# Kernel optimization log

Hardware: AMD Instinct MI355X
Metric: run time of the kernel (lower is better)

Reference implementation:

```python
import jax, jax.numpy as jnp
import numpy as np

N = 8192
EPS = 1e-7  # matches torch BCE's internal log clamping behavior


def setup_inputs() -> dict:
    key = jax.random.key(0)
    ks = jax.random.split(key, 8)
    return {
        "solar_score": jax.random.normal(ks[0], (N,), dtype=jnp.float32),
        "solar_ranking_gt": jax.random.randint(ks[1], (N,), 0, 1000000, dtype=jnp.int64),
        "capacity_pred": jax.random.normal(ks[2], (N,), dtype=jnp.float32),
        "capacity_gt": jax.random.normal(ks[3], (N,), dtype=jnp.float32),
        "roi_pred": jax.random.normal(ks[4], (N,), dtype=jnp.float32),
        "roi_gt": jax.random.normal(ks[5], (N,), dtype=jnp.float32),
        "viable_pred": jax.random.uniform(ks[6], (N,), dtype=jnp.float32, minval=1e-4, maxval=1.0 - 1e-4),
        "viable_gt": jax.random.uniform(ks[7], (N,), dtype=jnp.float32),
    }


def _pairwise_ranking_loss(scores, gt_ranking):
    n = scores.shape[0]
    # pair (i, j) with i < j contributes iff gt_ranking[i] < gt_ranking[j]
    upper = jnp.triu(jnp.ones((n, n), dtype=bool), k=1)
    mask = (gt_ranking[:, None] < gt_ranking[None, :]) & upper
    hinge = jax.nn.relu(1.0 - (scores[:, None] - scores[None, :]))  # [n, n]
    count = jnp.sum(mask)
    total = jnp.sum(jnp.where(mask, hinge, 0.0))
    return jnp.where(count > 0, total / count.astype(scores.dtype), jnp.zeros((), scores.dtype))


def reference(solar_score, solar_ranking_gt, capacity_pred, capacity_gt,
              roi_pred, roi_gt, viable_pred, viable_gt):
    ranking_loss = _pairwise_ranking_loss(solar_score, solar_ranking_gt)

    capacity_loss = jnp.mean((capacity_pred - capacity_gt) ** 2)

    d = roi_pred - roi_gt  # smooth_l1 with beta=1 (torch default)
    ad = jnp.abs(d)
    roi_loss = jnp.mean(jnp.where(ad < 1.0, 0.5 * d * d, ad - 0.5))

    p = jnp.clip(viable_pred, EPS, 1.0 - EPS)
    viability_loss = -jnp.mean(viable_gt * jnp.log(p) + (1.0 - viable_gt) * jnp.log1p(-p))

    return (ranking_loss + capacity_loss + roi_loss + viability_loss) / 4.0
```

## Files before the change

### kernel.cpp

```cpp
#include <hip/hip_runtime.h>

#define NELEM 8192
#define NPAIR 1024
#define NTHREADS 512
#define JTILE (NTHREADS * 4)
#define EPSV 1e-7f
#define TAG16   0xA5C3u
#define MAGIC32 0xA5C3F17Du

__global__ __launch_bounds__(NTHREADS, 4) void solar_fused_kernel(
    const float* __restrict__ s, const int* __restrict__ r,
    const float* __restrict__ cp, const float* __restrict__ cg,
    const float* __restrict__ rp, const float* __restrict__ rg,
    const float* __restrict__ vp, const float* __restrict__ vg,
    unsigned long long* __restrict__ pw, float* __restrict__ out) {

    const int b   = blockIdx.x;
    const int tid = threadIdx.x;

    __shared__ float    rft[NTHREADS / 64];
    __shared__ float    rfe[NTHREADS / 64];
    __shared__ unsigned rcu[NTHREADS / 64];
    __shared__ double   dd[NTHREADS / 64];
    __shared__ unsigned cc[NTHREADS / 64];
    __shared__ float    fe[NTHREADS / 64];

    const int joff = tid * 4;
    const int i0a = 4 * b;
    const int i0b = 8188 - 4 * b;

    const float4 sa4 = *reinterpret_cast<const float4*>(s + i0a);
    const int4   ra4 = *reinterpret_cast<const int4*>(r + i0a);
    const float4 sb4 = *reinterpret_cast<const float4*>(s + i0b);
    const int4   rb4 = *reinterpret_cast<const int4*>(r + i0b);
    const float4 c1a = make_float4(1.0f - sa4.x, 1.0f - sa4.y, 1.0f - sa4.z, 1.0f - sa4.w);
    const float4 c1b = make_float4(1.0f - sb4.x, 1.0f - sb4.y, 1.0f - sb4.z, 1.0f - sb4.w);

    float    tacc[4] = {0.0f, 0.0f, 0.0f, 0.0f};
    unsigned cnt_u   = 0;

    auto comp_full = [&](float4 sj, int4 rj, float4 c1, int4 ri) {
        const float c1e[4] = {c1.x, c1.y, c1.z, c1.w};
        const int   rie[4] = {ri.x, ri.y, ri.z, ri.w};
        const float sje[4] = {sj.x, sj.y, sj.z, sj.w};
        const int   rje[4] = {rj.x, rj.y, rj.z, rj.w};
#pragma unroll
        for (int k = 0; k < 4; ++k) {
#pragma unroll
            for (int e = 0; e < 4; ++e) {
                const bool cond = rie[k] < rje[e];
                const float h = fmaxf(0.0f, c1e[k] + sje[e]);
                tacc[e] += cond ? h : 0.0f;
                cnt_u += (unsigned)__popcll(__ballot(cond));
            }
        }
    };

    auto comp_diag = [&](float4 sj, int4 rj, float4 c1, int4 ri, int jb, int i0) {
        const float c1e[4] = {c1.x, c1.y, c1.z, c1.w};
        const int   rie[4] = {ri.x, ri.y, ri.z, ri.w};
        const float sje[4] = {sj.x, sj.y, sj.z, sj.w};
        const int   rje[4] = {rj.x, rj.y, rj.z, rj.w};
#pragma unroll
        for (int k = 0; k < 4; ++k) {
#pragma unroll
            for (int e = 0; e < 4; ++e) {
                const bool cond = ((jb + e) > (i0 + k)) & (rie[k] < rje[e]);
                const float h = fmaxf(0.0f, c1e[k] + sje[e]);
                tacc[e] += cond ? h : 0.0f;
                cnt_u += (unsigned)__popcll(__ballot(cond));
            }
        }
    };

    if (b < 512) {
        const int jb0 = joff, jb1 = JTILE + joff, jb2 = 2 * JTILE + joff, jb3 = 3 * JTILE + joff;
        const float4 s1 = *reinterpret_cast<const float4*>(s + jb1);
        const float4 s2 = *reinterpret_cast<const float4*>(s + jb2);
        const float4 s3 = *reinterpret_cast<const float4*>(s + jb3);
        const int4   r1 = *reinterpret_cast<const int4*>(r + jb1);
        const int4   r2 = *reinterpret_cast<const int4*>(r + jb2);
        const int4   r3 = *reinterpret_cast<const int4*>(r + jb3);

        comp_full(s1, r1, c1a, ra4);
        comp_full(s2, r2, c1a, ra4);
        comp_full(s3, r3, c1a, ra4);

        if (__any((jb0 + 3) > i0a)) {
            const float4 s0 = *reinterpret_cast<const float4*>(s + jb0);
            const int4   r0 = *reinterpret_cast<const int4*>(r + jb0);
            comp_diag(s0, r0, c1a, ra4, jb0, i0a);
        }
        if (__any((jb3 + 3) > i0b)) {
            comp_diag(s3, r3, c1b, rb4, jb3, i0b);
        }
    } else {
        const int jb1 = JTILE + joff, jb2 = 2 * JTILE + joff, jb3 = 3 * JTILE + joff;
        const float4 s2 = *reinterpret_cast<const float4*>(s + jb2);
        const float4 s3 = *reinterpret_cast<const float4*>(s + jb3);
        const int4   r2 = *reinterpret_cast<const int4*>(r + jb2);
        const int4   r3 = *reinterpret_cast<const int4*>(r + jb3);

        comp_full(s2, r2, c1a, ra4);
        comp_full(s3, r3, c1a, ra4);
        comp_full(s3, r3, c1b, rb4);

        if (__any((jb1 + 3) > i0a)) {
            const float4 s1 = *reinterpret_cast<const float4*>(s + jb1);
            const int4   r1 = *reinterpret_cast<const int4*>(r + jb1);
            comp_diag(s1, r1, c1a, ra4, jb1, i0a);
        }
        if (__any((jb2 + 3) > i0b)) {
            comp_diag(s2, r2, c1b, rb4, jb2, i0b);
        }
    }

    float ext = 0.0f;
    if (tid < 8) {
        const int i = b * 8 + tid;
        const float dc = cp[i] - cg[i];
        const float cap = dc * dc;
        const float dr = rp[i] - rg[i];
        const float ad = fabsf(dr);
        const float roi = (ad < 1.0f) ? 0.5f * dr * dr : (ad - 0.5f);
        const float p = fminf(fmaxf(vp[i], EPSV), 1.0f - EPSV);
        const float g = vg[i];
        const float bce = g * logf(p) + (1.0f - g) * log1pf(-p);
        ext = cap + roi - bce;
    }

    float tsum = (tacc[0] + tacc[1]) + (tacc[2] + tacc[3]);
#pragma unroll
    for (int off = 32; off > 0; off >>= 1) {
        tsum += __shfl_down(tsum, off);
        ext  += __shfl_down(ext,  off);
    }

    const int wave = tid >> 6;
    const int lane = tid & 63;
    if (lane == 0) { rft[wave] = tsum; rfe[wave] = ext; rcu[wave] = cnt_u; }
    __syncthreads();

    if (tid == 0) {
        float bt = 0.0f, be = 0.0f;
        unsigned bc = 0;
#pragma unroll
        for (int w = 0; w < NTHREADS / 64; ++w) { bt += rft[w]; be += rfe[w]; bc += rcu[w]; }
        const unsigned long long w0 =
            ((unsigned long long)((TAG16 << 16) | (bc & 0xFFFFu)) << 32) | (unsigned long long)__float_as_uint(bt);
        const unsigned long long w1 =
            ((unsigned long long)MAGIC32 << 32) | (unsigned long long)__float_as_uint(be);
        __hip_atomic_store(&pw[2 * b],     w0, __ATOMIC_RELAXED, __HIP_MEMORY_SCOPE_AGENT);
        __hip_atomic_store(&pw[2 * b + 1], w1, __ATOMIC_RELAXED, __HIP_MEMORY_SCOPE_AGENT);
    }

    if (b == 0) {
        double   td = 0.0;
        unsigned cn = 0;
        float    ex = 0.0f;
#pragma unroll
        for (int q = 0; q < 2; ++q) {
            const int blk = tid + q * NTHREADS;
            unsigned long long w0 = __hip_atomic_load(&pw[2 * blk], __ATOMIC_RELAXED, __HIP_MEMORY_SCOPE_AGENT);
            while ((unsigned)(w0 >> 48) != TAG16) {
                __builtin_amdgcn_s_sleep(2);
                w0 = __hip_atomic_load(&pw[2 * blk], __ATOMIC_RELAXED, __HIP_MEMORY_SCOPE_AGENT);
            }
            unsigned long long w1 = __hip_atomic_load(&pw[2 * blk + 1], __ATOMIC_RELAXED, __HIP_MEMORY_SCOPE_AGENT);
            while ((unsigned)(w1 >> 32) != MAGIC32) {
                __builtin_amdgcn_s_sleep(2);
                w1 = __hip_atomic_load(&pw[2 * blk + 1], __ATOMIC_RELAXED, __HIP_MEMORY_SCOPE_AGENT);
            }
            td += (double)__uint_as_float((unsigned)w0);
            cn += (unsigned)((w0 >> 32) & 0xFFFFu);
            ex += __uint_as_float((unsigned)w1);
        }

#pragma unroll
        for (int off = 32; off > 0; off >>= 1) {
            td += __shfl_down(td, off);
            cn += __shfl_down(cn, off);
            ex += __shfl_down(ex, off);
        }
        if (lane == 0) { dd[wave] = td; cc[wave] = cn; fe[wave] = ex; }
        __syncthreads();

        if (tid == 0) {
            double t = 0.0;
            unsigned long long c = 0;
            float e = 0.0f;
#pragma unroll
            for (int w = 0; w < NTHREADS / 64; ++w) { t += dd[w]; c += cc[w]; e += fe[w]; }
            const float rank = (c > 0) ? (float)(t / (double)c) : 0.0f;
            out[0] = 0.25f * rank + e * (0.25f / (float)NELEM);
        }
    }
}

extern "C" void kernel_launch(void* const* d_in, const int* in_sizes, int n_in,
                              void* d_out, int out_size, void* d_ws, size_t ws_size,
                              hipStream_t stream) {
    const float* s  = (const float*)d_in[0];
    const int*   r  = (const int*)d_in[1];
    const float* cp = (const float*)d_in[2];
    const float* cg = (const float*)d_in[3];
    const float* rp = (const float*)d_in[4];
    const float* rg = (const float*)d_in[5];
    const float* vp = (const float*)d_in[6];
    const float* vg = (const float*)d_in[7];
    float* out = (float*)d_out;
    unsigned long long* pw = (unsigned long long*)d_ws;

    solar_fused_kernel<<<NPAIR, NTHREADS, 0, stream>>>(s, r, cp, cg, rp, rg, vp, vg, pw, out);
}
```

Baseline: 12.19 us.

## Halve block count with 8 rows per block and packed-add hinge accumulation

Each block now handles 8 i-rows from each end of the triangle instead of 4, so 512 blocks replace 1024 and every loaded j-tile is reused across twice as many rows. The inner loop uses v_pk_add_f32 for the hinge sums and accumulates per-lane counts in integers, reducing them once via shuffles instead of a ballot/popcount per element. The workspace handshake is rebuilt with a new tag layout and an 18-bit count field, and the final block reads one entry per thread. The risks are higher register pressure at 512 threads, fewer blocks to cover the GPU, and correctness of the rewritten diagonal masking and count packing.

Measured after the change: 13.70 us. 12.3% more time.

```diff
diff --git a/kernel.cpp b/kernel.cpp
--- a/kernel.cpp
+++ b/kernel.cpp
@@ -1,12 +1,20 @@
 #include <hip/hip_runtime.h>
 
 #define NELEM 8192
-#define NPAIR 1024
+#define NBLK 512
 #define NTHREADS 512
-#define JTILE (NTHREADS * 4)
+#define JTILE 2048
 #define EPSV 1e-7f
-#define TAG16   0xA5C3u
 #define MAGIC32 0xA5C3F17Du
+#define TAG14   0x25C3u
+
+typedef float f32x2 __attribute__((ext_vector_type(2)));
+
+__device__ __forceinline__ f32x2 pk_add(f32x2 a, f32x2 b) {
+    f32x2 d;
+    asm("v_pk_add_f32 %0, %1, %2" : "=v"(d) : "v"(a), "v"(b));
+    return d;
+}
 
 __global__ __launch_bounds__(NTHREADS, 4) void solar_fused_kernel(
     const float* __restrict__ s, const int* __restrict__ r,
@@ -26,55 +34,84 @@
     __shared__ float    fe[NTHREADS / 64];
 
     const int joff = tid * 4;
-    const int i0a = 4 * b;
-    const int i0b = 8188 - 4 * b;
-
-    const float4 sa4 = *reinterpret_cast<const float4*>(s + i0a);
-    const int4   ra4 = *reinterpret_cast<const int4*>(r + i0a);
-    const float4 sb4 = *reinterpret_cast<const float4*>(s + i0b);
-    const int4   rb4 = *reinterpret_cast<const int4*>(r + i0b);
-    const float4 c1a = make_float4(1.0f - sa4.x, 1.0f - sa4.y, 1.0f - sa4.z, 1.0f - sa4.w);
-    const float4 c1b = make_float4(1.0f - sb4.x, 1.0f - sb4.y, 1.0f - sb4.z, 1.0f - sb4.w);
-
-    float    tacc[4] = {0.0f, 0.0f, 0.0f, 0.0f};
-    unsigned cnt_u   = 0;
-
-    auto comp_full = [&](float4 sj, int4 rj, float4 c1, int4 ri) {
-        const float c1e[4] = {c1.x, c1.y, c1.z, c1.w};
-        const int   rie[4] = {ri.x, ri.y, ri.z, ri.w};
-        const float sje[4] = {sj.x, sj.y, sj.z, sj.w};
-        const int   rje[4] = {rj.x, rj.y, rj.z, rj.w};
-#pragma unroll
-        for (int k = 0; k < 4; ++k) {
-#pragma unroll
-            for (int e = 0; e < 4; ++e) {
-                const bool cond = rie[k] < rje[e];
-                const float h = fmaxf(0.0f, c1e[k] + sje[e]);
-                tacc[e] += cond ? h : 0.0f;
-                cnt_u += (unsigned)__popcll(__ballot(cond));
-            }
+    const int i0a = 8 * b;
+    const int i0b = 8184 - 8 * b;
+
+    const float4 sa0 = *reinterpret_cast<const float4*>(s + i0a);
+    const float4 sa1 = *reinterpret_cast<const float4*>(s + i0a + 4);
+    const int4   ra0 = *reinterpret_cast<const int4*>(r + i0a);
+    const int4   ra1 = *reinterpret_cast<const int4*>(r + i0a + 4);
+    const float4 sb0 = *reinterpret_cast<const float4*>(s + i0b);
+    const float4 sb1 = *reinterpret_cast<const float4*>(s + i0b + 4);
+    const int4   rb0 = *reinterpret_cast<const int4*>(r + i0b);
+    const int4   rb1 = *reinterpret_cast<const int4*>(r + i0b + 4);
+
+    f32x2 c1pA[8]; int riA[8];
+    f32x2 c1pB[8]; int riB[8];
+    {
+        const float ca[8] = {1.0f - sa0.x, 1.0f - sa0.y, 1.0f - sa0.z, 1.0f - sa0.w,
+                             1.0f - sa1.x, 1.0f - sa1.y, 1.0f - sa1.z, 1.0f - sa1.w};
+        const float cb[8] = {1.0f - sb0.x, 1.0f - sb0.y, 1.0f - sb0.z, 1.0f - sb0.w,
+                             1.0f - sb1.x, 1.0f - sb1.y, 1.0f - sb1.z, 1.0f - sb1.w};
+        const int ia[8] = {ra0.x, ra0.y, ra0.z, ra0.w, ra1.x, ra1.y, ra1.z, ra1.w};
+        const int ib[8] = {rb0.x, rb0.y, rb0.z, rb0.w, rb1.x, rb1.y, rb1.z, rb1.w};
+#pragma unroll
+        for (int k = 0; k < 8; ++k) {
+            c1pA[k] = (f32x2){ca[k], ca[k]}; riA[k] = ia[k];
+            c1pB[k] = (f32x2){cb[k], cb[k]}; riB[k] = ib[k];
+        }
+    }
+
+    f32x2 acc01 = (f32x2){0.0f, 0.0f};
+    f32x2 acc23 = (f32x2){0.0f, 0.0f};
+    int cacc0 = 0, cacc1 = 0, cacc2 = 0, cacc3 = 0;
+
+    auto comp_full = [&](float4 sj, int4 rj, const f32x2* c1p, const int* ri) {
+        const f32x2 sj01 = (f32x2){sj.x, sj.y};
+        const f32x2 sj23 = (f32x2){sj.z, sj.w};
+#pragma unroll
+        for (int k = 0; k < 8; ++k) {
+            const f32x2 x01 = pk_add(c1p[k], sj01);
+            const f32x2 x23 = pk_add(c1p[k], sj23);
+            const bool c0 = ri[k] < rj.x;
+            const bool c1 = ri[k] < rj.y;
+            const bool c2 = ri[k] < rj.z;
+            const bool c3 = ri[k] < rj.w;
+            f32x2 hm01, hm23;
+            hm01.x = c0 ? fmaxf(0.0f, x01.x) : 0.0f;
+            hm01.y = c1 ? fmaxf(0.0f, x01.y) : 0.0f;
+            hm23.x = c2 ? fmaxf(0.0f, x23.x) : 0.0f;
+            hm23.y = c3 ? fmaxf(0.0f, x23.y) : 0.0f;
+            acc01 = pk_add(acc01, hm01);
+            acc23 = pk_add(acc23, hm23);
+            cacc0 += c0; cacc1 += c1; cacc2 += c2; cacc3 += c3;
         }
     };
 
-    auto comp_diag = [&](float4 sj, int4 rj, float4 c1, int4 ri, int jb, int i0) {
-        const float c1e[4] = {c1.x, c1.y, c1.z, c1.w};
-        const int   rie[4] = {ri.x, ri.y, ri.z, ri.w};
-        const float sje[4] = {sj.x, sj.y, sj.z, sj.w};
-        const int   rje[4] = {rj.x, rj.y, rj.z, rj.w};
-#pragma unroll
-        for (int k = 0; k < 4; ++k) {
-#pragma unroll
-            for (int e = 0; e < 4; ++e) {
-                const bool cond = ((jb + e) > (i0 + k)) & (rie[k] < rje[e]);
-                const float h = fmaxf(0.0f, c1e[k] + sje[e]);
-                tacc[e] += cond ? h : 0.0f;
-                cnt_u += (unsigned)__popcll(__ballot(cond));
-            }
+    auto comp_diag = [&](float4 sj, int4 rj, const f32x2* c1p, const int* ri, int dA) {
+        const f32x2 sj01 = (f32x2){sj.x, sj.y};
+        const f32x2 sj23 = (f32x2){sj.z, sj.w};
+#pragma unroll
+        for (int k = 0; k < 8; ++k) {
+            const f32x2 x01 = pk_add(c1p[k], sj01);
+            const f32x2 x23 = pk_add(c1p[k], sj23);
+            const bool c0 = (dA > k)     & (ri[k] < rj.x);
+            const bool c1 = (dA > k - 1) & (ri[k] < rj.y);
+            const bool c2 = (dA > k - 2) & (ri[k] < rj.z);
+            const bool c3 = (dA > k - 3) & (ri[k] < rj.w);
+            f32x2 hm01, hm23;
+            hm01.x = c0 ? fmaxf(0.0f, x01.x) : 0.0f;
+            hm01.y = c1 ? fmaxf(0.0f, x01.y) : 0.0f;
+            hm23.x = c2 ? fmaxf(0.0f, x23.x) : 0.0f;
+            hm23.y = c3 ? fmaxf(0.0f, x23.y) : 0.0f;
+            acc01 = pk_add(acc01, hm01);
+            acc23 = pk_add(acc23, hm23);
+            cacc0 += c0; cacc1 += c1; cacc2 += c2; cacc3 += c3;
         }
     };
 
-    if (b < 512) {
-        const int jb0 = joff, jb1 = JTILE + joff, jb2 = 2 * JTILE + joff, jb3 = 3 * JTILE + joff;
+    if (b < 256) {
+        const int jb1 = JTILE + joff, jb2 = 2 * JTILE + joff, jb3 = 3 * JTILE + joff;
         const float4 s1 = *reinterpret_cast<const float4*>(s + jb1);
         const float4 s2 = *reinterpret_cast<const float4*>(s + jb2);
         const float4 s3 = *reinterpret_cast<const float4*>(s + jb3);
@@ -82,18 +119,18 @@
         const int4   r2 = *reinterpret_cast<const int4*>(r + jb2);
         const int4   r3 = *reinterpret_cast<const int4*>(r + jb3);
 
-        comp_full(s1, r1, c1a, ra4);
-        comp_full(s2, r2, c1a, ra4);
-        comp_full(s3, r3, c1a, ra4);
-
-        if (__any((jb0 + 3) > i0a)) {
-            const float4 s0 = *reinterpret_cast<const float4*>(s + jb0);
-            const int4   r0 = *reinterpret_cast<const int4*>(r + jb0);
-            comp_diag(s0, r0, c1a, ra4, jb0, i0a);
-        }
-        if (__any((jb3 + 3) > i0b)) {
-            comp_diag(s3, r3, c1b, rb4, jb3, i0b);
-        }
+        comp_full(s1, r1, c1pA, riA);
+        comp_full(s2, r2, c1pA, riA);
+        comp_full(s3, r3, c1pA, riA);
+
+        const int dA0 = joff - i0a;
+        if (dA0 > -3) {
+            const float4 s0 = *reinterpret_cast<const float4*>(s + joff);
+            const int4   r0 = *reinterpret_cast<const int4*>(r + joff);
+            comp_diag(s0, r0, c1pA, riA, dA0);
+        }
+        const int dB3 = jb3 - i0b;
+        if (dB3 > -3) comp_diag(s3, r3, c1pB, riB, dB3);
     } else {
         const int jb1 = JTILE + joff, jb2 = 2 * JTILE + joff, jb3 = 3 * JTILE + joff;
         const float4 s2 = *reinterpret_cast<const float4*>(s + jb2);
@@ -101,23 +138,23 @@
         const int4   r2 = *reinterpret_cast<const int4*>(r + jb2);
         const int4   r3 = *reinterpret_cast<const int4*>(r + jb3);
 
-        comp_full(s2, r2, c1a, ra4);
-        comp_full(s3, r3, c1a, ra4);
-        comp_full(s3, r3, c1b, rb4);
-
-        if (__any((jb1 + 3) > i0a)) {
+        comp_full(s2, r2, c1pA, riA);
+        comp_full(s3, r3, c1pA, riA);
+        comp_full(s3, r3, c1pB, riB);
+
+        const int dA1 = jb1 - i0a;
+        if (dA1 > -3) {
             const float4 s1 = *reinterpret_cast<const float4*>(s + jb1);
             const int4   r1 = *reinterpret_cast<const int4*>(r + jb1);
-            comp_diag(s1, r1, c1a, ra4, jb1, i0a);
-        }
-        if (__any((jb2 + 3) > i0b)) {
-            comp_diag(s2, r2, c1b, rb4, jb2, i0b);
-        }
+            comp_diag(s1, r1, c1pA, riA, dA1);
+        }
+        const int dB2 = jb2 - i0b;
+        if (dB2 > -3) comp_diag(s2, r2, c1pB, riB, dB2);
     }
 
     float ext = 0.0f;
-    if (tid < 8) {
-        const int i = b * 8 + tid;
+    if (tid < 16) {
+        const int i = b * 16 + tid;
         const float dc = cp[i] - cg[i];
         const float cap = dc * dc;
         const float dr = rp[i] - rg[i];
@@ -129,52 +166,49 @@
         ext = cap + roi - bce;
     }
 
-    float tsum = (tacc[0] + tacc[1]) + (tacc[2] + tacc[3]);
+    float    tsum = (acc01.x + acc01.y) + (acc23.x + acc23.y);
+    unsigned cnti = (unsigned)((cacc0 + cacc1) + (cacc2 + cacc3));
+
 #pragma unroll
     for (int off = 32; off > 0; off >>= 1) {
         tsum += __shfl_down(tsum, off);
+        cnti += __shfl_down(cnti, off);
         ext  += __shfl_down(ext,  off);
     }
 
     const int wave = tid >> 6;
     const int lane = tid & 63;
-    if (lane == 0) { rft[wave] = tsum; rfe[wave] = ext; rcu[wave] = cnt_u; }
+    if (lane == 0) { rft[wave] = tsum; rcu[wave] = cnti; rfe[wave] = ext; }
     __syncthreads();
 
     if (tid == 0) {
         float bt = 0.0f, be = 0.0f;
         unsigned bc = 0;
 #pragma unroll
-        for (int w = 0; w < NTHREADS / 64; ++w) { bt += rft[w]; be += rfe[w]; bc += rcu[w]; }
+        for (int w = 0; w < NTHREADS / 64; ++w) { bt += rft[w]; bc += rcu[w]; be += rfe[w]; }
         const unsigned long long w0 =
-            ((unsigned long long)((TAG16 << 16) | (bc & 0xFFFFu)) << 32) | (unsigned long long)__float_as_uint(bt);
+            ((unsigned long long)MAGIC32 << 32) | (unsigned long long)__float_as_uint(bt);
         const unsigned long long w1 =
-            ((unsigned long long)MAGIC32 << 32) | (unsigned long long)__float_as_uint(be);
+            (((unsigned long long)((TAG14 << 18) | (bc & 0x3FFFFu))) << 32) | (unsigned long long)__float_as_uint(be);
         __hip_atomic_store(&pw[2 * b],     w0, __ATOMIC_RELAXED, __HIP_MEMORY_SCOPE_AGENT);
         __hip_atomic_store(&pw[2 * b + 1], w1, __ATOMIC_RELAXED, __HIP_MEMORY_SCOPE_AGENT);
     }
 
     if (b == 0) {
-        double   td = 0.0;
-        unsigned cn = 0;
-        float    ex = 0.0f;
-#pragma unroll
-        for (int q = 0; q < 2; ++q) {
-            const int blk = tid + q * NTHREADS;
-            unsigned long long w0 = __hip_atomic_load(&pw[2 * blk], __ATOMIC_RELAXED, __HIP_MEMORY_SCOPE_AGENT);
-            while ((unsigned)(w0 >> 48) != TAG16) {
-                __builtin_amdgcn_s_sleep(2);
-                w0 = __hip_atomic_load(&pw[2 * blk], __ATOMIC_RELAXED, __HIP_MEMORY_SCOPE_AGENT);
-            }
-            unsigned long long w1 = __hip_atomic_load(&pw[2 * blk + 1], __ATOMIC_RELAXED, __HIP_MEMORY_SCOPE_AGENT);
-            while ((unsigned)(w1 >> 32) != MAGIC32) {
-                __builtin_amdgcn_s_sleep(2);
-                w1 = __hip_atomic_load(&pw[2 * blk + 1], __ATOMIC_RELAXED, __HIP_MEMORY_SCOPE_AGENT);
-            }
-            td += (double)__uint_as_float((unsigned)w0);
-            cn += (unsigned)((w0 >> 32) & 0xFFFFu);
-            ex += __uint_as_float((unsigned)w1);
-        }
+        unsigned long long w0 = __hip_atomic_load(&pw[2 * tid], __ATOMIC_RELAXED, __HIP_MEMORY_SCOPE_AGENT);
+        while ((unsigned)(w0 >> 32) != MAGIC32) {
+            __builtin_amdgcn_s_sleep(2);
+            w0 = __hip_atomic_load(&pw[2 * tid], __ATOMIC_RELAXED, __HIP_MEMORY_SCOPE_AGENT);
+        }
+        unsigned long long w1 = __hip_atomic_load(&pw[2 * tid + 1], __ATOMIC_RELAXED, __HIP_MEMORY_SCOPE_AGENT);
+        while ((unsigned)(w1 >> 50) != TAG14) {
+            __builtin_amdgcn_s_sleep(2);
+            w1 = __hip_atomic_load(&pw[2 * tid + 1], __ATOMIC_RELAXED, __HIP_MEMORY_SCOPE_AGENT);
+        }
+
+        double   td = (double)__uint_as_float((unsigned)w0);
+        unsigned cn = (unsigned)((w1 >> 32) & 0x3FFFFu);
+        float    ex = __uint_as_float((unsigned)w1);
 
 #pragma unroll
         for (int off = 32; off > 0; off >>= 1) {
@@ -211,5 +245,5 @@
     float* out = (float*)d_out;
     unsigned long long* pw = (unsigned long long*)d_ws;
 
-    solar_fused_kernel<<<NPAIR, NTHREADS, 0, stream>>>(s, r, cp, cg, rp, rg, vp, vg, pw, out);
+    solar_fused_kernel<<<NBLK, NTHREADS, 0, stream>>>(s, r, cp, cg, rp, rg, vp, vg, pw, out);
 }
```
